# Kernel optimization log

Measured on AMD Instinct MI355X. Metric: run time of the kernel, lower is better.

The kernel has to match this reference:

```python
import jax, jax.numpy as jnp
import numpy as np

B, T, C, H = 2, 2048, 1024, 16
N = C // H
MISS_ROWS = 128


def _rwkv7_scan(q, w_log, k, v, a, b):
    # all [B,T,H,N] float32 (bf16-rounded). RWKV7 delta-rule recurrence:
    #   S_t = S_{t-1} * diag(exp(w_t)) + (S_{t-1} a_t) b_t^T + v_t k_t^T
    #   o_t = S_t q_t   (state S has shape [B,H,Nv,Nk]; decay along k-dim)
    Bq, Tq, Hq, Nq = q.shape

    def step(S, inp):
        q_t, w_t, k_t, v_t, a_t, b_t = inp
        ew = jnp.exp(w_t)  # decay in (0,1) since w_log = -exp(...) < 0
        sa = jnp.einsum('bhvi,bhi->bhv', S, a_t)
        S = S * ew[:, :, None, :] + sa[..., None] * b_t[:, :, None, :] + v_t[..., None] * k_t[:, :, None, :]
        o = jnp.einsum('bhvj,bhj->bhv', S, q_t)
        return S, o

    xs = tuple(jnp.moveaxis(u, 1, 0) for u in (q, w_log, k, v, a, b))
    S0 = jnp.zeros((Bq, Hq, Nq, Nq), jnp.float32)
    _, o = jax.lax.scan(step, S0, xs)
    return jnp.moveaxis(o, 0, 1)  # [B,T,H,N]


def setup_inputs() -> dict:
    key = jax.random.key(0)
    ks = jax.random.split(key, 16)
    f32 = jnp.float32
    return {
        'residual': jax.random.normal(ks[0], (B, T, C), f32),
        'x': jax.random.normal(ks[1], (B, T, C), f32),
        'x0': jax.random.normal(ks[2], (B, T, C), f32),
        'dx0': jax.random.normal(ks[3], (B, T, C), f32),
        'Wq': jax.random.normal(ks[4], (C, C), f32) * 0.02,
        'Wk': jax.random.normal(ks[5], (C, C), f32) * 0.02,
        'Wv': jax.random.normal(ks[6], (C, C), f32) * 0.02,
        'Wproj': jax.random.normal(ks[7], (C, C), f32) * 0.02,
        'x_q': jax.random.uniform(ks[8], (1, 1, C), f32),
        'x_k': jax.random.uniform(ks[9], (1, 1, C), f32),
        'x_v': jax.random.uniform(ks[10], (1, 1, C), f32),
        'v0': 0.7 + 0.1 * jax.random.normal(ks[11], (1, 1, C), f32),
        'w0': -3.0 + 0.5 * jax.random.normal(ks[12], (1, 1, C), f32),
        'a0': 0.1 * jax.random.normal(ks[13], (1, 1, C), f32),
        'miss': jax.random.normal(ks[14], (MISS_ROWS, 4 * C), f32) * 0.02,
        'r_k': 0.1 * jax.random.normal(ks[15], (H, N), f32),
    }


def reference(residual, x, x0, dx0, Wq, Wk, Wv, Wproj, x_q, x_k, x_v, v0, w0, a0, miss, r_k):
    Bx, Tx, Cx = x.shape
    Hh, Nn = r_k.shape
    # token shift: dx_prev = x_{t-1} - x_t (zero-padded at t=0)
    dx_prev = jnp.concatenate([jnp.zeros_like(x[:, :1]), x[:, :-1]], axis=1) - x
    q = (x + dx_prev * x_q) @ Wq.T
    k = (x + dx_prev * x_k) @ Wk.T
    v = (x + dx_prev * x_v) @ Wv.T
    deltas = x[:, :, :miss.shape[0]] @ miss  # [B,T,4C]
    w_delta, v_delta, a_delta, g = jnp.split(deltas, 4, axis=-1)
    log_neglog_w = -jax.nn.softplus(-(w0 + w_delta)) - 0.5
    log_w = -jnp.exp(log_neglog_w)  # log decay, always < 0
    v_first = (x0 + dx0 * x_v) @ Wv.T
    v = v + (v_first - v) * jax.nn.sigmoid(v0 + v_delta)
    g = 1.0 + g
    a = jax.nn.sigmoid(a0 + a_delta)
    kh = k.reshape(Bx, Tx, Hh, Nn)
    kk = kh / jnp.maximum(jnp.linalg.norm(kh, axis=-1, keepdims=True), 1e-12)
    kk = kk.reshape(Bx, Tx, Cx)
    k = k * a
    z = -kk
    b = kk * a
    bf = lambda u: u.astype(jnp.bfloat16).astype(jnp.float32).reshape(Bx, Tx, Hh, Nn)
    qh, wh, kh2, vh, zh, bh = (bf(u) for u in (q, log_w, k, v, z, b))
    y = _rwkv7_scan(qh, wh, kh2, vh, zh, bh) * (float(Nn) ** -0.5)  # [B,T,H,N]
    xnorm = jnp.linalg.norm(x.reshape(Bx, Tx, Hh, Nn), axis=-1, keepdims=True)
    vnorm = jnp.linalg.norm(vh, axis=-1, keepdims=True)
    u = (1.0 - xnorm / (vnorm + 1e-12)) * jax.nn.sigmoid(r_k)
    y = (y + vh * u).reshape(Bx, Tx, Cx)
    y = y * g
    return residual + y @ Wproj.T
```

## Files before the change

### kernel.cpp

```cpp
#include <hip/hip_runtime.h>
#include <stdint.h>
#include <stddef.h>

#define B_ 2
#define T_ 2048
#define C_ 1024
#define H_ 16
#define N_ 64
#define M_ (B_*T_)
#define L_ 128
#define NC_ (T_/L_)

typedef unsigned short ushort_t;
typedef __attribute__((ext_vector_type(8))) __bf16 bf16x8;
typedef __attribute__((ext_vector_type(4))) float  f32x4;

__device__ __forceinline__ ushort_t f2bf(float x){
  uint32_t u = __float_as_uint(x);
  u += 0x7fffu + ((u >> 16) & 1u);
  return (ushort_t)(u >> 16);
}
__device__ __forceinline__ float bf2f(uint32_t hu){
  return __uint_as_float(hu << 16);
}

__device__ __forceinline__ ushort4 mixq4(float4 a, float4 p, float4 c){
  ushort4 o;
  o.x = f2bf(fmaf(p.x - a.x, c.x, a.x));
  o.y = f2bf(fmaf(p.y - a.y, c.y, a.y));
  o.z = f2bf(fmaf(p.z - a.z, c.z, a.z));
  o.w = f2bf(fmaf(p.w - a.w, c.w, a.w));
  return o;
}
__global__ __launch_bounds__(256) void prep_act(
    const float* __restrict__ x, const float* __restrict__ x0,
    const float* __restrict__ dx0,
    const float* __restrict__ xq, const float* __restrict__ xk,
    const float* __restrict__ xv,
    ushort_t* __restrict__ Aq, ushort_t* __restrict__ Ak,
    ushort_t* __restrict__ Av, ushort_t* __restrict__ Axf,
    ushort_t* __restrict__ Xb)
{
  const int idx = blockIdx.x*256 + threadIdx.x;
  const int col4 = idx & 255;
  const int i = idx >> 8;
  const int t = i & (T_-1);
  float4 a = ((const float4*)x)[idx];
  float4 p = {0.f,0.f,0.f,0.f};
  if (t > 0) p = ((const float4*)x)[idx - 256];
  float4 cq = ((const float4*)xq)[col4];
  float4 ck = ((const float4*)xk)[col4];
  float4 cv = ((const float4*)xv)[col4];
  ((ushort4*)Aq)[idx] = mixq4(a, p, cq);
  ((ushort4*)Ak)[idx] = mixq4(a, p, ck);
  ((ushort4*)Av)[idx] = mixq4(a, p, cv);
  float4 z = ((const float4*)x0)[idx];
  float4 d = ((const float4*)dx0)[idx];
  ushort4 of;
  of.x = f2bf(fmaf(d.x, cv.x, z.x));
  of.y = f2bf(fmaf(d.y, cv.y, z.y));
  of.z = f2bf(fmaf(d.z, cv.z, z.z));
  of.w = f2bf(fmaf(d.w, cv.w, z.w));
  ((ushort4*)Axf)[idx] = of;
  ushort4 ob = {f2bf(a.x), f2bf(a.y), f2bf(a.z), f2bf(a.w)};
  ((ushort4*)Xb)[idx] = ob;
}

__global__ __launch_bounds__(256) void prep_w(
    const float* __restrict__ Wq, const float* __restrict__ Wk,
    const float* __restrict__ Wv, const float* __restrict__ Wp,
    ushort_t* __restrict__ Wb, ushort_t* __restrict__ Wpb)
{
  const int y = blockIdx.y;
  const float* src = (y==0)?Wq:(y==1)?Wk:(y<4)?Wv:Wp;
  ushort_t* dst = (y<4) ? Wb + (size_t)y*C_*C_ : Wpb;
  const int idx = blockIdx.x*256 + threadIdx.x;
  float4 v = ((const float4*)src)[idx];
  ushort4 o = {f2bf(v.x), f2bf(v.y), f2bf(v.z), f2bf(v.w)};
  ((ushort4*)dst)[idx] = o;
}

__global__ __launch_bounds__(256) void prep_missT(
    const float* __restrict__ miss, ushort_t* __restrict__ missT)
{
  __shared__ ushort_t tile[128][66];
  const int j0 = blockIdx.x*64;
  const int tid = threadIdx.x;
#pragma unroll
  for (int rep=0; rep<8; rep++){
    int k = rep*16 + (tid>>4);
    int jj = (tid&15)*4;
    float4 v = *(const float4*)&miss[(size_t)k*4096 + j0 + jj];
    tile[k][jj+0]=f2bf(v.x); tile[k][jj+1]=f2bf(v.y);
    tile[k][jj+2]=f2bf(v.z); tile[k][jj+3]=f2bf(v.w);
  }
  __syncthreads();
#pragma unroll
  for (int rep=0; rep<8; rep++){
    int j = tid>>2;
    int kk = (tid&3)*32 + rep*4;
    ushort4 o = {tile[kk+0][j], tile[kk+1][j], tile[kk+2][j], tile[kk+3][j]};
    *(ushort4*)&missT[(size_t)(j0+j)*128 + kk] = o;
  }
}

__global__ __launch_bounds__(256, 2) void mfma_gemm(
    const ushort_t* __restrict__ Ab, int lda, int64_t Asz,
    const ushort_t* __restrict__ Bbp, int ldb, int64_t Bsz,
    void* __restrict__ Cb, int ldc, int64_t Csz, int c_bf16,
    const float* __restrict__ resid, int K)
{
  const ushort_t* A  = Ab  + (size_t)blockIdx.z * Asz;
  const ushort_t* Bm = Bbp + (size_t)blockIdx.z * Bsz;
  const int i0 = blockIdx.y * 128;
  const int j0 = blockIdx.x * 128;
  const int tid = threadIdx.x;
  const int lane = tid & 63;
  const int w = tid >> 6;
  const int wm = w & 1, wn = w >> 1;

  __shared__ ushort_t As[128*32];
  __shared__ ushort_t Bs[128*32];

  f32x4 acc[4][4];
#pragma unroll
  for (int i=0;i<4;i++)
#pragma unroll
    for (int j=0;j<4;j++) acc[i][j] = (f32x4){0.f,0.f,0.f,0.f};

  const int lr = lane >> 2;
  const int ls = lane & 3;
  const ushort_t* ga = A  + (size_t)(i0 + w*32 + lr)*lda + ls*8;
  const ushort_t* gb = Bm + (size_t)(j0 + w*32 + lr)*ldb + ls*8;
  const int lm = lane & 15, lq = lane >> 4;

  for (int k0 = 0; k0 < K; k0 += 32){
    __syncthreads();
#pragma unroll
    for (int p=0;p<2;p++){
      __builtin_amdgcn_global_load_lds(
        (const __attribute__((address_space(1))) void*)(ga + (size_t)p*16*lda + k0),
        (__attribute__((address_space(3))) void*)&As[(w*32 + p*16)*32], 16, 0, 0);
      __builtin_amdgcn_global_load_lds(
        (const __attribute__((address_space(1))) void*)(gb + (size_t)p*16*ldb + k0),
        (__attribute__((address_space(3))) void*)&Bs[(w*32 + p*16)*32], 16, 0, 0);
    }
    __syncthreads();
    bf16x8 af[4], bfr[4];
#pragma unroll
    for (int i=0;i<4;i++)
      af[i] = *(const bf16x8*)&As[(wm*64 + i*16 + lm)*32 + lq*8];
#pragma unroll
    for (int j=0;j<4;j++)
      bfr[j] = *(const bf16x8*)&Bs[(wn*64 + j*16 + lm)*32 + lq*8];
#pragma unroll
    for (int i=0;i<4;i++)
#pragma unroll
      for (int j=0;j<4;j++)
        acc[i][j] = __builtin_amdgcn_mfma_f32_16x16x32_bf16(af[i], bfr[j], acc[i][j], 0, 0, 0);
  }

  if (!c_bf16){
    float* C = (float*)Cb + (size_t)blockIdx.z * Csz;
#pragma unroll
    for (int i=0;i<4;i++)
#pragma unroll
      for (int j=0;j<4;j++)
#pragma unroll
        for (int r=0;r<4;r++){
          const int row = i0 + wm*64 + i*16 + lq*4 + r;
          const int col = j0 + wn*64 + j*16 + lm;
          float v = acc[i][j][r];
          if (resid) v += resid[(size_t)row*ldc + col];
          C[(size_t)row*ldc + col] = v;
        }
  } else {
    ushort_t* C = (ushort_t*)Cb + (size_t)blockIdx.z * Csz;
#pragma unroll
    for (int i=0;i<4;i++)
#pragma unroll
      for (int j=0;j<4;j++)
#pragma unroll
        for (int r=0;r<4;r++){
          const int row = i0 + wm*64 + i*16 + lq*4 + r;
          const int col = j0 + wn*64 + j*16 + lm;
          C[(size_t)row*ldc + col] = f2bf(acc[i][j][r]);
        }
  }
}

__global__ __launch_bounds__(256) void fuse_kernel(
    const float* __restrict__ qm, const float* __restrict__ km,
    const float* __restrict__ vm, const float* __restrict__ vfm,
    const ushort_t* __restrict__ del, const float* __restrict__ x,
    const float* __restrict__ w0, const float* __restrict__ v0,
    const float* __restrict__ a0,
    uint32_t* __restrict__ packed, float* __restrict__ gout,
    float* __restrict__ ratio)
{
  const int lane = threadIdx.x & 63;
  const int ht = blockIdx.x*4 + (threadIdx.x >> 6);
  const int i = ht >> 4;
  const int h = ht & 15;
  const int c = h*64 + lane;
  const size_t ic = (size_t)i*C_ + c;
  float qv = qm[ic], kv = km[ic], vv = vm[ic], vfv = vfm[ic], xv = x[ic];
  const size_t d0 = (size_t)i*4*C_ + c;
  float wd = bf2f(del[d0]), vd = bf2f(del[d0+C_]);
  float ad = bf2f(del[d0+2*C_]), gd = bf2f(del[d0+3*C_]);

  float z1 = -(w0[c]+wd);
  float sp = fmaxf(z1, 0.f) + log1pf(expf(-fabsf(z1)));
  float logw = -expf(-sp - 0.5f);
  float sv = 1.f/(1.f+expf(-(v0[c]+vd)));
  vv = vv + (vfv - vv)*sv;
  float gv = 1.f + gd;
  float av = 1.f/(1.f+expf(-(a0[c]+ad)));

  ushort_t vr_u = f2bf(vv);
  float vrf = bf2f(vr_u);

  float ksq = kv*kv, xsq = xv*xv, vsq = vrf*vrf;
#pragma unroll
  for (int off=32; off>0; off>>=1){
    ksq += __shfl_xor(ksq, off, 64);
    xsq += __shfl_xor(xsq, off, 64);
    vsq += __shfl_xor(vsq, off, 64);
  }
  float kn = sqrtf(ksq);
  float kkn = kv / fmaxf(kn, 1e-12f);
  float k2 = kv*av;
  float zv = -kkn;
  float bv = kkn*av;

  uint32_t p0 = (uint32_t)f2bf(logw) | ((uint32_t)f2bf(zv) << 16);
  uint32_t p1 = (uint32_t)f2bf(bv)   | ((uint32_t)f2bf(k2) << 16);
  uint32_t p2 = (uint32_t)f2bf(qv)   | ((uint32_t)vr_u << 16);
  uint32_t* pb = packed + ((size_t)ht*64 + lane)*3;
  pb[0]=p0; pb[1]=p1; pb[2]=p2;
  gout[ic] = gv;
  if (lane == 0)
    ratio[ht] = 1.f - sqrtf(xsq)/(sqrtf(vsq)+1e-12f);
}


__global__ __launch_bounds__(256) void chunk_phi_kernel(
    const uint32_t* __restrict__ packed,
    float* __restrict__ phi, float* __restrict__ cc)
{
  const int blk = blockIdx.x;
  const int c  = blk & (NC_-1);
  const int bh = blk >> 4;
  const int b = bh >> 4, h = bh & 15;
  const int tid = threadIdx.x;
  const int rp = tid >> 2;
  const int qr = tid & 3;
  const int t0 = c * L_;

  __shared__ float ewS[4][N_], zS[4][N_], bS[4][N_], kS[4][N_], vS[4][N_];

  float X[16], Z[16];
#pragma unroll
  for (int i=0;i<16;i++){ X[i] = (qr*16+i == rp) ? 1.f : 0.f; Z[i] = 0.f; }

  const int s = tid >> 6, d = tid & 63;
  size_t ap = (((size_t)(b*T_+t0+s))*H_ + h)*64 + d;
  uint32_t pu0 = packed[ap*3], pu1 = packed[ap*3+1], pu2 = packed[ap*3+2];

  for (int tg = 0; tg < L_; tg += 4){
    __syncthreads();
    ewS[s][d] = __expf(bf2f(pu0 & 0xffffu));
    zS[s][d]  = bf2f(pu0 >> 16);
    bS[s][d]  = bf2f(pu1 & 0xffffu);
    kS[s][d]  = bf2f(pu1 >> 16);
    vS[s][d]  = bf2f(pu2 >> 16);
    if (tg + 4 < L_){
      size_t a2 = (((size_t)(b*T_+t0+tg+4+s))*H_ + h)*64 + d;
      pu0 = packed[a2*3]; pu1 = packed[a2*3+1]; pu2 = packed[a2*3+2];
    }
    __syncthreads();
#pragma unroll 1
    for (int ss=0; ss<4; ss++){
      float4 zv[4], ev[4], bv4[4], kv[4];
#pragma unroll
      for (int i4=0;i4<4;i4++){
        zv[i4]  = *(const float4*)&zS[ss][qr*16+i4*4];
        ev[i4]  = *(const float4*)&ewS[ss][qr*16+i4*4];
        bv4[i4] = *(const float4*)&bS[ss][qr*16+i4*4];
        kv[i4]  = *(const float4*)&kS[ss][qr*16+i4*4];
      }
      const float vr = vS[ss][rp];
      float a0=0.f,a1=0.f,a2=0.f,a3=0.f, c0=0.f,c1=0.f,c2=0.f,c3=0.f;
#pragma unroll
      for (int i4=0;i4<4;i4++){
        const float4 z4 = zv[i4];
        a0 = fmaf(X[i4*4+0], z4.x, a0); a1 = fmaf(X[i4*4+1], z4.y, a1);
        a2 = fmaf(X[i4*4+2], z4.z, a2); a3 = fmaf(X[i4*4+3], z4.w, a3);
        c0 = fmaf(Z[i4*4+0], z4.x, c0); c1 = fmaf(Z[i4*4+1], z4.y, c1);
        c2 = fmaf(Z[i4*4+2], z4.z, c2); c3 = fmaf(Z[i4*4+3], z4.w, c3);
      }
      float sx = (a0+a1)+(a2+a3);
      float sz = (c0+c1)+(c2+c3);
      sx += __shfl_xor(sx,1,64); sx += __shfl_xor(sx,2,64);
      sz += __shfl_xor(sz,1,64); sz += __shfl_xor(sz,2,64);
#pragma unroll
      for (int i4=0;i4<4;i4++){
        const float4 e4=ev[i4], b4=bv4[i4], k4=kv[i4];
        X[i4*4+0] = fmaf(X[i4*4+0], e4.x, sx*b4.x);
        X[i4*4+1] = fmaf(X[i4*4+1], e4.y, sx*b4.y);
        X[i4*4+2] = fmaf(X[i4*4+2], e4.z, sx*b4.z);
        X[i4*4+3] = fmaf(X[i4*4+3], e4.w, sx*b4.w);
        Z[i4*4+0] = fmaf(Z[i4*4+0], e4.x, fmaf(sz, b4.x, vr*k4.x));
        Z[i4*4+1] = fmaf(Z[i4*4+1], e4.y, fmaf(sz, b4.y, vr*k4.y));
        Z[i4*4+2] = fmaf(Z[i4*4+2], e4.z, fmaf(sz, b4.z, vr*k4.z));
        Z[i4*4+3] = fmaf(Z[i4*4+3], e4.w, fmaf(sz, b4.w, vr*k4.w));
      }
    }
  }
  const size_t base = (size_t)blk*4096 + (size_t)rp*64 + qr*16;
#pragma unroll
  for (int i4=0;i4<4;i4++){
    float4 xo = {X[i4*4+0],X[i4*4+1],X[i4*4+2],X[i4*4+3]};
    float4 zo = {Z[i4*4+0],Z[i4*4+1],Z[i4*4+2],Z[i4*4+3]};
    *(float4*)&phi[base + i4*4] = xo;
    *(float4*)&cc [base + i4*4] = zo;
  }
}

__global__ __launch_bounds__(256) void chunk_state_kernel(
    const float* __restrict__ phi, const float* __restrict__ cc,
    float* __restrict__ sstart)
{
  const int bh = blockIdx.x;
  const int tid = threadIdx.x;
  const int rb = tid >> 4;
  const int cq = tid & 15;
  __shared__ float Sld[64][65];
  __shared__ float Fld[64][68];
  float acc[4][4];
#pragma unroll
  for (int m=0;m<4;m++)
#pragma unroll
    for (int i=0;i<4;i++) acc[m][i] = 0.f;
#pragma unroll
  for (int m=0;m<4;m++){
    float4 z4 = {0.f,0.f,0.f,0.f};
    *(float4*)&Sld[rb+16*m][cq*4] = z4;
  }
  const float* pc = phi + (size_t)bh*NC_*4096;
  float4 pf[4];
#pragma unroll
  for (int p=0;p<4;p++) pf[p] = *(const float4*)&pc[(size_t)p*1024 + tid*4];

  for (int c=0;c<NC_;c++){
    __syncthreads();
#pragma unroll
    for (int p=0;p<4;p++){
      int f = p*1024 + tid*4;
      *(float4*)&Fld[f>>6][f&63] = pf[p];
    }
    if (c+1 < NC_){
#pragma unroll
      for (int p=0;p<4;p++) pf[p] = *(const float4*)&pc[(size_t)(c+1)*4096 + p*1024 + tid*4];
    }
    float na[4][4];
#pragma unroll
    for (int m=0;m<4;m++){
      float4 ci = *(const float4*)&cc[(size_t)(bh*NC_+c)*4096 + (size_t)(rb+16*m)*64 + cq*4];
      na[m][0]=ci.x; na[m][1]=ci.y; na[m][2]=ci.z; na[m][3]=ci.w;
    }
#pragma unroll
    for (int m=0;m<4;m++){
      float4 so = {acc[m][0],acc[m][1],acc[m][2],acc[m][3]};
      *(float4*)&sstart[(size_t)(bh*NC_+c)*4096 + (size_t)(rb+16*m)*64 + cq*4] = so;
    }
    __syncthreads();
#pragma unroll 1
    for (int k0=0;k0<64;k0+=4){
      float4 sr[4];
#pragma unroll
      for (int m=0;m<4;m++) sr[m] = *(const float4*)&Sld[rb+16*m][k0];
      const float4 f0 = *(const float4*)&Fld[k0+0][cq*4];
      const float4 f1 = *(const float4*)&Fld[k0+1][cq*4];
      const float4 f2 = *(const float4*)&Fld[k0+2][cq*4];
      const float4 f3 = *(const float4*)&Fld[k0+3][cq*4];
#pragma unroll
      for (int m=0;m<4;m++){
        na[m][0] = fmaf(sr[m].x, f0.x, na[m][0]); na[m][0] = fmaf(sr[m].y, f1.x, na[m][0]);
        na[m][0] = fmaf(sr[m].z, f2.x, na[m][0]); na[m][0] = fmaf(sr[m].w, f3.x, na[m][0]);
        na[m][1] = fmaf(sr[m].x, f0.y, na[m][1]); na[m][1] = fmaf(sr[m].y, f1.y, na[m][1]);
        na[m][1] = fmaf(sr[m].z, f2.y, na[m][1]); na[m][1] = fmaf(sr[m].w, f3.y, na[m][1]);
        na[m][2] = fmaf(sr[m].x, f0.z, na[m][2]); na[m][2] = fmaf(sr[m].y, f1.z, na[m][2]);
        na[m][2] = fmaf(sr[m].z, f2.z, na[m][2]); na[m][2] = fmaf(sr[m].w, f3.z, na[m][2]);
        na[m][3] = fmaf(sr[m].x, f0.w, na[m][3]); na[m][3] = fmaf(sr[m].y, f1.w, na[m][3]);
        na[m][3] = fmaf(sr[m].z, f2.w, na[m][3]); na[m][3] = fmaf(sr[m].w, f3.w, na[m][3]);
      }
    }
    __syncthreads();
#pragma unroll
    for (int m=0;m<4;m++){
      float4 so = {na[m][0],na[m][1],na[m][2],na[m][3]};
      *(float4*)&Sld[rb+16*m][cq*4] = so;
#pragma unroll
      for (int i=0;i<4;i++) acc[m][i] = na[m][i];
    }
  }
}

__global__ __launch_bounds__(256) void chunk_out_kernel(
    const uint32_t* __restrict__ packed, const float* __restrict__ ratio,
    const float* __restrict__ g, const float* __restrict__ rk,
    const float* __restrict__ sstart, ushort_t* __restrict__ y)
{
  const int blk = blockIdx.x;
  const int c  = blk & (NC_-1);
  const int bh = blk >> 4;
  const int b = bh >> 4, h = bh & 15;
  const int tid = threadIdx.x;
  const int r  = tid >> 2;
  const int qr = tid & 3;
  const int t0 = c * L_;

  __shared__ float ewS[4][N_], zS[4][N_], bS[4][N_], kS[4][N_], qS[4][N_], vS[4][N_], gS[4][N_];
  __shared__ float ratS[4];

  float S[16];
#pragma unroll
  for (int i4=0;i4<4;i4++){
    float4 s4 = *(const float4*)&sstart[(size_t)blk*4096 + (size_t)r*64 + qr*16 + i4*4];
    S[i4*4+0]=s4.x; S[i4*4+1]=s4.y; S[i4*4+2]=s4.z; S[i4*4+3]=s4.w;
  }
  const float sigrk = 1.f/(1.f+__expf(-rk[h*64+r]));

  const int s = tid >> 6, d = tid & 63;
  size_t ap = (((size_t)(b*T_+t0+s))*H_ + h)*64 + d;
  uint32_t pu0 = packed[ap*3], pu1 = packed[ap*3+1], pu2 = packed[ap*3+2];
  float pg = g[(size_t)(b*T_+t0+s)*C_ + h*64 + d];
  float prat = 0.f;
  if (d == 0) prat = ratio[(size_t)(b*T_+t0+s)*H_ + h];

  for (int tg = 0; tg < L_; tg += 4){
    __syncthreads();
    ewS[s][d] = __expf(bf2f(pu0 & 0xffffu));
    zS[s][d]  = bf2f(pu0 >> 16);
    bS[s][d]  = bf2f(pu1 & 0xffffu);
    kS[s][d]  = bf2f(pu1 >> 16);
    qS[s][d]  = bf2f(pu2 & 0xffffu);
    vS[s][d]  = bf2f(pu2 >> 16);
    gS[s][d]  = pg;
    if (d == 0) ratS[s] = prat;
    if (tg + 4 < L_){
      size_t a2 = (((size_t)(b*T_+t0+tg+4+s))*H_ + h)*64 + d;
      pu0 = packed[a2*3]; pu1 = packed[a2*3+1]; pu2 = packed[a2*3+2];
      pg = g[(size_t)(b*T_+t0+tg+4+s)*C_ + h*64 + d];
      if (d == 0) prat = ratio[(size_t)(b*T_+t0+tg+4+s)*H_ + h];
    }
    __syncthreads();
#pragma unroll 1
    for (int ss=0; ss<4; ss++){
      float4 zv[4], ev[4], bv4[4], kv[4], qv[4];
#pragma unroll
      for (int i4=0;i4<4;i4++){
        zv[i4]  = *(const float4*)&zS[ss][qr*16+i4*4];
        ev[i4]  = *(const float4*)&ewS[ss][qr*16+i4*4];
        bv4[i4] = *(const float4*)&bS[ss][qr*16+i4*4];
        kv[i4]  = *(const float4*)&kS[ss][qr*16+i4*4];
        qv[i4]  = *(const float4*)&qS[ss][qr*16+i4*4];
      }
      const float vr = vS[ss][r];
      const float gvr = gS[ss][r];
      const float uv = ratS[ss];
      float a0=0.f,a1=0.f,a2=0.f,a3=0.f;
#pragma unroll
      for (int i4=0;i4<4;i4++){
        const float4 z4 = zv[i4];
        a0 = fmaf(S[i4*4+0], z4.x, a0); a1 = fmaf(S[i4*4+1], z4.y, a1);
        a2 = fmaf(S[i4*4+2], z4.z, a2); a3 = fmaf(S[i4*4+3], z4.w, a3);
      }
      float sa = (a0+a1)+(a2+a3);
      sa += __shfl_xor(sa,1,64); sa += __shfl_xor(sa,2,64);
      float p0=0.f,p1=0.f,p2=0.f,p3=0.f;
#pragma unroll
      for (int i4=0;i4<4;i4++){
        const float4 e4=ev[i4], b4=bv4[i4], k4=kv[i4], q4=qv[i4];
        float t;
        t = fmaf(S[i4*4+0], e4.x, fmaf(sa, b4.x, vr*k4.x)); S[i4*4+0]=t; p0 = fmaf(t, q4.x, p0);
        t = fmaf(S[i4*4+1], e4.y, fmaf(sa, b4.y, vr*k4.y)); S[i4*4+1]=t; p1 = fmaf(t, q4.y, p1);
        t = fmaf(S[i4*4+2], e4.z, fmaf(sa, b4.z, vr*k4.z)); S[i4*4+2]=t; p2 = fmaf(t, q4.z, p2);
        t = fmaf(S[i4*4+3], e4.w, fmaf(sa, b4.w, vr*k4.w)); S[i4*4+3]=t; p3 = fmaf(t, q4.w, p3);
      }
      float o = (p0+p1)+(p2+p3);
      o += __shfl_xor(o,1,64); o += __shfl_xor(o,2,64);
      if (qr == 0){
        y[(size_t)(b*T_+t0+tg+ss)*C_ + h*64 + r] = f2bf((o*0.125f + vr*uv*sigrk)*gvr);
      }
    }
  }
}

extern "C" void kernel_launch(void* const* d_in, const int* in_sizes, int n_in,
                              void* d_out, int out_size, void* d_ws, size_t ws_size,
                              hipStream_t stream)
{
  const float* residual = (const float*)d_in[0];
  const float* x    = (const float*)d_in[1];
  const float* x0   = (const float*)d_in[2];
  const float* dx0  = (const float*)d_in[3];
  const float* Wq   = (const float*)d_in[4];
  const float* Wk   = (const float*)d_in[5];
  const float* Wv   = (const float*)d_in[6];
  const float* Wpr  = (const float*)d_in[7];
  const float* x_q  = (const float*)d_in[8];
  const float* x_k  = (const float*)d_in[9];
  const float* x_v  = (const float*)d_in[10];
  const float* v0   = (const float*)d_in[11];
  const float* w0   = (const float*)d_in[12];
  const float* a0   = (const float*)d_in[13];
  const float* miss = (const float*)d_in[14];
  const float* rk   = (const float*)d_in[15];
  float* out = (float*)d_out;

  char* ws = (char*)d_ws;
  const size_t MB = (size_t)1 << 20;
  float*    q_m    = (float*)(ws + 0*MB);
  float*    k_m    = (float*)(ws + 16*MB);
  float*    v_m    = (float*)(ws + 32*MB);
  float*    vf_m   = (float*)(ws + 48*MB);
  ushort_t* delb   = (ushort_t*)(ws + 64*MB);
  float*    phi    = (float*)(ws + 96*MB);
  float*    cc     = (float*)(ws + 104*MB);
  float*    sstart = (float*)(ws + 112*MB);
  ushort_t* Wpb    = (ushort_t*)(ws + 120*MB);
  ushort_t* missT  = (ushort_t*)(ws + 122*MB);
  ushort_t* Ab     = (ushort_t*)(ws + 124*MB);
  ushort_t* Xb     = (ushort_t*)(ws + 156*MB);
  ushort_t* Wb     = (ushort_t*)(ws + 164*MB);
  uint32_t* packed = (uint32_t*)(ws + 124*MB);
  float*    g_m    = (float*)(ws + 172*MB);
  float*    ratio  = (float*)(ws + 188*MB);
  ushort_t* yb     = (ushort_t*)(ws + 0*MB);

  ushort_t* Aq  = Ab + 0*(size_t)M_*C_;
  ushort_t* Ak  = Ab + 1*(size_t)M_*C_;
  ushort_t* Av  = Ab + 2*(size_t)M_*C_;
  ushort_t* Axf = Ab + 3*(size_t)M_*C_;

  dim3 blk(256);
  prep_act<<<M_*C_/4/256, blk, 0, stream>>>(x, x0, dx0, x_q, x_k, x_v, Aq, Ak, Av, Axf, Xb);
  prep_w<<<dim3(C_*C_/4/256, 5), blk, 0, stream>>>(Wq, Wk, Wv, Wpr, Wb, Wpb);
  prep_missT<<<4096/64, blk, 0, stream>>>(miss, missT);
  mfma_gemm<<<dim3(C_/128, M_/128, 4), blk, 0, stream>>>(
      Ab, C_, (int64_t)M_*C_, Wb, C_, (int64_t)C_*C_,
      q_m, C_, (int64_t)M_*C_, 0, nullptr, C_);
  mfma_gemm<<<dim3(4*C_/128, M_/128, 1), blk, 0, stream>>>(
      Xb, C_, 0, missT, 128, 0, delb, 4*C_, 0, 1, nullptr, 128);
  fuse_kernel<<<M_*H_/4, blk, 0, stream>>>(q_m, k_m, v_m, vf_m, delb, x, w0, v0, a0, packed, g_m, ratio);
  chunk_phi_kernel<<<B_*H_*NC_, blk, 0, stream>>>(packed, phi, cc);
  chunk_state_kernel<<<B_*H_, blk, 0, stream>>>(phi, cc, sstart);
  chunk_out_kernel<<<B_*H_*NC_, blk, 0, stream>>>(packed, ratio, g_m, rk, sstart, yb);
  mfma_gemm<<<dim3(C_/128, M_/128, 1), blk, 0, stream>>>(
      yb, C_, 0, Wpb, C_, 0, out, C_, 0, 0, residual, C_);
}
```

Baseline: 531.0 us.

## Precompute chunk-local output projections so emit pass is parallel dot products

The chunk pass now also records, per timestep, the projections of the affine state maps onto q (md buffer). The output stage becomes an embarrassingly parallel dot product of the chunk start state with these vectors, replacing the second sequential recurrence. The chunk length is halved to give more parallel blocks, and the three prep kernels are merged into one launch. The cost is extra global traffic for the md buffer and a longer sequential state-propagation chain across twice as many chunks.

```diff
diff --git a/kernel.cpp b/kernel.cpp
--- a/kernel.cpp
+++ b/kernel.cpp
@@ -8,7 +8,7 @@
 #define H_ 16
 #define N_ 64
 #define M_ (B_*T_)
-#define L_ 128
+#define L_ 64
 #define NC_ (T_/L_)
 
 typedef unsigned short ushort_t;
@@ -32,75 +32,73 @@
   o.w = f2bf(fmaf(p.w - a.w, c.w, a.w));
   return o;
 }
-__global__ __launch_bounds__(256) void prep_act(
+__global__ __launch_bounds__(256) void prep_all(
     const float* __restrict__ x, const float* __restrict__ x0,
     const float* __restrict__ dx0,
     const float* __restrict__ xq, const float* __restrict__ xk,
     const float* __restrict__ xv,
+    const float* __restrict__ Wq, const float* __restrict__ Wk,
+    const float* __restrict__ Wv, const float* __restrict__ Wp,
+    const float* __restrict__ miss,
     ushort_t* __restrict__ Aq, ushort_t* __restrict__ Ak,
     ushort_t* __restrict__ Av, ushort_t* __restrict__ Axf,
-    ushort_t* __restrict__ Xb)
-{
-  const int idx = blockIdx.x*256 + threadIdx.x;
-  const int col4 = idx & 255;
-  const int i = idx >> 8;
-  const int t = i & (T_-1);
-  float4 a = ((const float4*)x)[idx];
-  float4 p = {0.f,0.f,0.f,0.f};
-  if (t > 0) p = ((const float4*)x)[idx - 256];
-  float4 cq = ((const float4*)xq)[col4];
-  float4 ck = ((const float4*)xk)[col4];
-  float4 cv = ((const float4*)xv)[col4];
-  ((ushort4*)Aq)[idx] = mixq4(a, p, cq);
-  ((ushort4*)Ak)[idx] = mixq4(a, p, ck);
-  ((ushort4*)Av)[idx] = mixq4(a, p, cv);
-  float4 z = ((const float4*)x0)[idx];
-  float4 d = ((const float4*)dx0)[idx];
-  ushort4 of;
-  of.x = f2bf(fmaf(d.x, cv.x, z.x));
-  of.y = f2bf(fmaf(d.y, cv.y, z.y));
-  of.z = f2bf(fmaf(d.z, cv.z, z.z));
-  of.w = f2bf(fmaf(d.w, cv.w, z.w));
-  ((ushort4*)Axf)[idx] = of;
-  ushort4 ob = {f2bf(a.x), f2bf(a.y), f2bf(a.z), f2bf(a.w)};
-  ((ushort4*)Xb)[idx] = ob;
-}
-
-__global__ __launch_bounds__(256) void prep_w(
-    const float* __restrict__ Wq, const float* __restrict__ Wk,
-    const float* __restrict__ Wv, const float* __restrict__ Wp,
-    ushort_t* __restrict__ Wb, ushort_t* __restrict__ Wpb)
-{
-  const int y = blockIdx.y;
-  const float* src = (y==0)?Wq:(y==1)?Wk:(y<4)?Wv:Wp;
-  ushort_t* dst = (y<4) ? Wb + (size_t)y*C_*C_ : Wpb;
-  const int idx = blockIdx.x*256 + threadIdx.x;
-  float4 v = ((const float4*)src)[idx];
-  ushort4 o = {f2bf(v.x), f2bf(v.y), f2bf(v.z), f2bf(v.w)};
-  ((ushort4*)dst)[idx] = o;
-}
-
-__global__ __launch_bounds__(256) void prep_missT(
-    const float* __restrict__ miss, ushort_t* __restrict__ missT)
+    ushort_t* __restrict__ Xb,
+    ushort_t* __restrict__ Wb, ushort_t* __restrict__ Wpb,
+    ushort_t* __restrict__ missT)
 {
   __shared__ ushort_t tile[128][66];
-  const int j0 = blockIdx.x*64;
+  const int blk = blockIdx.x;
   const int tid = threadIdx.x;
-#pragma unroll
-  for (int rep=0; rep<8; rep++){
-    int k = rep*16 + (tid>>4);
-    int jj = (tid&15)*4;
-    float4 v = *(const float4*)&miss[(size_t)k*4096 + j0 + jj];
-    tile[k][jj+0]=f2bf(v.x); tile[k][jj+1]=f2bf(v.y);
-    tile[k][jj+2]=f2bf(v.z); tile[k][jj+3]=f2bf(v.w);
-  }
-  __syncthreads();
-#pragma unroll
-  for (int rep=0; rep<8; rep++){
-    int j = tid>>2;
-    int kk = (tid&3)*32 + rep*4;
-    ushort4 o = {tile[kk+0][j], tile[kk+1][j], tile[kk+2][j], tile[kk+3][j]};
-    *(ushort4*)&missT[(size_t)(j0+j)*128 + kk] = o;
+  if (blk < 4096){
+    const int idx = blk*256 + tid;
+    const int col4 = idx & 255;
+    const int i = idx >> 8;
+    const int t = i & (T_-1);
+    float4 a = ((const float4*)x)[idx];
+    float4 p = {0.f,0.f,0.f,0.f};
+    if (t > 0) p = ((const float4*)x)[idx - 256];
+    float4 cq = ((const float4*)xq)[col4];
+    float4 ck = ((const float4*)xk)[col4];
+    float4 cv = ((const float4*)xv)[col4];
+    ((ushort4*)Aq)[idx] = mixq4(a, p, cq);
+    ((ushort4*)Ak)[idx] = mixq4(a, p, ck);
+    ((ushort4*)Av)[idx] = mixq4(a, p, cv);
+    float4 z = ((const float4*)x0)[idx];
+    float4 d = ((const float4*)dx0)[idx];
+    ushort4 of;
+    of.x = f2bf(fmaf(d.x, cv.x, z.x));
+    of.y = f2bf(fmaf(d.y, cv.y, z.y));
+    of.z = f2bf(fmaf(d.z, cv.z, z.z));
+    of.w = f2bf(fmaf(d.w, cv.w, z.w));
+    ((ushort4*)Axf)[idx] = of;
+    ushort4 ob = {f2bf(a.x), f2bf(a.y), f2bf(a.z), f2bf(a.w)};
+    ((ushort4*)Xb)[idx] = ob;
+  } else if (blk < 4096 + 5*1024){
+    const int y = (blk - 4096) >> 10;
+    const float* src = (y==0)?Wq:(y==1)?Wk:(y<4)?Wv:Wp;
+    ushort_t* dst = (y<4) ? Wb + (size_t)y*C_*C_ : Wpb;
+    const int idx = ((blk - 4096) & 1023)*256 + tid;
+    float4 v = ((const float4*)src)[idx];
+    ushort4 o = {f2bf(v.x), f2bf(v.y), f2bf(v.z), f2bf(v.w)};
+    ((ushort4*)dst)[idx] = o;
+  } else {
+    const int j0 = (blk - 4096 - 5*1024)*64;
+#pragma unroll
+    for (int rep=0; rep<8; rep++){
+      int k = rep*16 + (tid>>4);
+      int jj = (tid&15)*4;
+      float4 v = *(const float4*)&miss[(size_t)k*4096 + j0 + jj];
+      tile[k][jj+0]=f2bf(v.x); tile[k][jj+1]=f2bf(v.y);
+      tile[k][jj+2]=f2bf(v.z); tile[k][jj+3]=f2bf(v.w);
+    }
+    __syncthreads();
+#pragma unroll
+    for (int rep=0; rep<8; rep++){
+      int j = tid>>2;
+      int kk = (tid&3)*32 + rep*4;
+      ushort4 o = {tile[kk+0][j], tile[kk+1][j], tile[kk+2][j], tile[kk+3][j]};
+      *(ushort4*)&missT[(size_t)(j0+j)*128 + kk] = o;
+    }
   }
 }
 
@@ -244,20 +242,20 @@
 }
 
 
-__global__ __launch_bounds__(256) void chunk_phi_kernel(
+__global__ __launch_bounds__(256) void chunk_mdp_kernel(
     const uint32_t* __restrict__ packed,
-    float* __restrict__ phi, float* __restrict__ cc)
+    float* __restrict__ phi, float* __restrict__ cc, float* __restrict__ md)
 {
   const int blk = blockIdx.x;
   const int c  = blk & (NC_-1);
-  const int bh = blk >> 4;
+  const int bh = blk >> 5;
   const int b = bh >> 4, h = bh & 15;
   const int tid = threadIdx.x;
   const int rp = tid >> 2;
   const int qr = tid & 3;
   const int t0 = c * L_;
 
-  __shared__ float ewS[4][N_], zS[4][N_], bS[4][N_], kS[4][N_], vS[4][N_];
+  __shared__ float ewS[4][N_], zS[4][N_], bS[4][N_], kS[4][N_], qS[4][N_], vS[4][N_];
 
   float X[16], Z[16];
 #pragma unroll
@@ -273,6 +271,7 @@
     zS[s][d]  = bf2f(pu0 >> 16);
     bS[s][d]  = bf2f(pu1 & 0xffffu);
     kS[s][d]  = bf2f(pu1 >> 16);
+    qS[s][d]  = bf2f(pu2 & 0xffffu);
     vS[s][d]  = bf2f(pu2 >> 16);
     if (tg + 4 < L_){
       size_t a2 = (((size_t)(b*T_+t0+tg+4+s))*H_ + h)*64 + d;
@@ -281,13 +280,14 @@
     __syncthreads();
 #pragma unroll 1
     for (int ss=0; ss<4; ss++){
-      float4 zv[4], ev[4], bv4[4], kv[4];
+      float4 zv[4], ev[4], bv4[4], kv[4], qv[4];
 #pragma unroll
       for (int i4=0;i4<4;i4++){
         zv[i4]  = *(const float4*)&zS[ss][qr*16+i4*4];
         ev[i4]  = *(const float4*)&ewS[ss][qr*16+i4*4];
         bv4[i4] = *(const float4*)&bS[ss][qr*16+i4*4];
         kv[i4]  = *(const float4*)&kS[ss][qr*16+i4*4];
+        qv[i4]  = *(const float4*)&qS[ss][qr*16+i4*4];
       }
       const float vr = vS[ss][rp];
       float a0=0.f,a1=0.f,a2=0.f,a3=0.f, c0=0.f,c1=0.f,c2=0.f,c3=0.f;
@@ -303,18 +303,26 @@
       float sz = (c0+c1)+(c2+c3);
       sx += __shfl_xor(sx,1,64); sx += __shfl_xor(sx,2,64);
       sz += __shfl_xor(sz,1,64); sz += __shfl_xor(sz,2,64);
+      float m0=0.f,m1=0.f,m2=0.f,m3=0.f, d0=0.f,d1=0.f,d2=0.f,d3=0.f;
 #pragma unroll
       for (int i4=0;i4<4;i4++){
-        const float4 e4=ev[i4], b4=bv4[i4], k4=kv[i4];
-        X[i4*4+0] = fmaf(X[i4*4+0], e4.x, sx*b4.x);
-        X[i4*4+1] = fmaf(X[i4*4+1], e4.y, sx*b4.y);
-        X[i4*4+2] = fmaf(X[i4*4+2], e4.z, sx*b4.z);
-        X[i4*4+3] = fmaf(X[i4*4+3], e4.w, sx*b4.w);
-        Z[i4*4+0] = fmaf(Z[i4*4+0], e4.x, fmaf(sz, b4.x, vr*k4.x));
-        Z[i4*4+1] = fmaf(Z[i4*4+1], e4.y, fmaf(sz, b4.y, vr*k4.y));
-        Z[i4*4+2] = fmaf(Z[i4*4+2], e4.z, fmaf(sz, b4.z, vr*k4.z));
-        Z[i4*4+3] = fmaf(Z[i4*4+3], e4.w, fmaf(sz, b4.w, vr*k4.w));
+        const float4 e4=ev[i4], b4=bv4[i4], k4=kv[i4], q4=qv[i4];
+        float t;
+        t = fmaf(X[i4*4+0], e4.x, sx*b4.x); X[i4*4+0]=t; m0 = fmaf(t, q4.x, m0);
+        t = fmaf(X[i4*4+1], e4.y, sx*b4.y); X[i4*4+1]=t; m1 = fmaf(t, q4.y, m1);
+        t = fmaf(X[i4*4+2], e4.z, sx*b4.z); X[i4*4+2]=t; m2 = fmaf(t, q4.z, m2);
+        t = fmaf(X[i4*4+3], e4.w, sx*b4.w); X[i4*4+3]=t; m3 = fmaf(t, q4.w, m3);
+        t = fmaf(Z[i4*4+0], e4.x, fmaf(sz, b4.x, vr*k4.x)); Z[i4*4+0]=t; d0 = fmaf(t, q4.x, d0);
+        t = fmaf(Z[i4*4+1], e4.y, fmaf(sz, b4.y, vr*k4.y)); Z[i4*4+1]=t; d1 = fmaf(t, q4.y, d1);
+        t = fmaf(Z[i4*4+2], e4.z, fmaf(sz, b4.z, vr*k4.z)); Z[i4*4+2]=t; d2 = fmaf(t, q4.z, d2);
+        t = fmaf(Z[i4*4+3], e4.w, fmaf(sz, b4.w, vr*k4.w)); Z[i4*4+3]=t; d3 = fmaf(t, q4.w, d3);
       }
+      float mv = (m0+m1)+(m2+m3);
+      float dv = (d0+d1)+(d2+d3);
+      mv += __shfl_xor(mv,1,64); mv += __shfl_xor(mv,2,64);
+      dv += __shfl_xor(dv,1,64); dv += __shfl_xor(dv,2,64);
+      if (qr == 0)      md[((size_t)blk*L_ + tg+ss)*128 + rp]      = mv;
+      else if (qr == 1) md[((size_t)blk*L_ + tg+ss)*128 + 64 + rp] = dv;
     }
   }
   const size_t base = (size_t)blk*4096 + (size_t)rp*64 + qr*16;
@@ -407,94 +415,48 @@
   }
 }
 
-__global__ __launch_bounds__(256) void chunk_out_kernel(
+__global__ __launch_bounds__(256) void chunk_emit_kernel(
     const uint32_t* __restrict__ packed, const float* __restrict__ ratio,
     const float* __restrict__ g, const float* __restrict__ rk,
-    const float* __restrict__ sstart, ushort_t* __restrict__ y)
+    const float* __restrict__ sstart, const float* __restrict__ md,
+    ushort_t* __restrict__ y)
 {
   const int blk = blockIdx.x;
   const int c  = blk & (NC_-1);
-  const int bh = blk >> 4;
+  const int bh = blk >> 5;
   const int b = bh >> 4, h = bh & 15;
   const int tid = threadIdx.x;
-  const int r  = tid >> 2;
-  const int qr = tid & 3;
-  const int t0 = c * L_;
-
-  __shared__ float ewS[4][N_], zS[4][N_], bS[4][N_], kS[4][N_], qS[4][N_], vS[4][N_], gS[4][N_];
-  __shared__ float ratS[4];
-
-  float S[16];
-#pragma unroll
-  for (int i4=0;i4<4;i4++){
-    float4 s4 = *(const float4*)&sstart[(size_t)blk*4096 + (size_t)r*64 + qr*16 + i4*4];
-    S[i4*4+0]=s4.x; S[i4*4+1]=s4.y; S[i4*4+2]=s4.z; S[i4*4+3]=s4.w;
-  }
-  const float sigrk = 1.f/(1.f+__expf(-rk[h*64+r]));
-
-  const int s = tid >> 6, d = tid & 63;
-  size_t ap = (((size_t)(b*T_+t0+s))*H_ + h)*64 + d;
-  uint32_t pu0 = packed[ap*3], pu1 = packed[ap*3+1], pu2 = packed[ap*3+2];
-  float pg = g[(size_t)(b*T_+t0+s)*C_ + h*64 + d];
-  float prat = 0.f;
-  if (d == 0) prat = ratio[(size_t)(b*T_+t0+s)*H_ + h];
-
-  for (int tg = 0; tg < L_; tg += 4){
-    __syncthreads();
-    ewS[s][d] = __expf(bf2f(pu0 & 0xffffu));
-    zS[s][d]  = bf2f(pu0 >> 16);
-    bS[s][d]  = bf2f(pu1 & 0xffffu);
-    kS[s][d]  = bf2f(pu1 >> 16);
-    qS[s][d]  = bf2f(pu2 & 0xffffu);
-    vS[s][d]  = bf2f(pu2 >> 16);
-    gS[s][d]  = pg;
-    if (d == 0) ratS[s] = prat;
-    if (tg + 4 < L_){
-      size_t a2 = (((size_t)(b*T_+t0+tg+4+s))*H_ + h)*64 + d;
-      pu0 = packed[a2*3]; pu1 = packed[a2*3+1]; pu2 = packed[a2*3+2];
-      pg = g[(size_t)(b*T_+t0+tg+4+s)*C_ + h*64 + d];
-      if (d == 0) prat = ratio[(size_t)(b*T_+t0+tg+4+s)*H_ + h];
-    }
-    __syncthreads();
+  const int v = tid & 63;
+  const int tg = tid >> 6;
+
+  float4 sr[16];
+  const float4* sp = (const float4*)(sstart + (size_t)blk*4096 + (size_t)v*64);
+#pragma unroll
+  for (int f=0;f<16;f++) sr[f] = sp[f];
+  const float sigrk = 1.f/(1.f+__expf(-rk[h*64+v]));
+
 #pragma unroll 1
-    for (int ss=0; ss<4; ss++){
-      float4 zv[4], ev[4], bv4[4], kv[4], qv[4];
-#pragma unroll
-      for (int i4=0;i4<4;i4++){
-        zv[i4]  = *(const float4*)&zS[ss][qr*16+i4*4];
-        ev[i4]  = *(const float4*)&ewS[ss][qr*16+i4*4];
-        bv4[i4] = *(const float4*)&bS[ss][qr*16+i4*4];
-        kv[i4]  = *(const float4*)&kS[ss][qr*16+i4*4];
-        qv[i4]  = *(const float4*)&qS[ss][qr*16+i4*4];
-      }
-      const float vr = vS[ss][r];
-      const float gvr = gS[ss][r];
-      const float uv = ratS[ss];
-      float a0=0.f,a1=0.f,a2=0.f,a3=0.f;
-#pragma unroll
-      for (int i4=0;i4<4;i4++){
-        const float4 z4 = zv[i4];
-        a0 = fmaf(S[i4*4+0], z4.x, a0); a1 = fmaf(S[i4*4+1], z4.y, a1);
-        a2 = fmaf(S[i4*4+2], z4.z, a2); a3 = fmaf(S[i4*4+3], z4.w, a3);
-      }
-      float sa = (a0+a1)+(a2+a3);
-      sa += __shfl_xor(sa,1,64); sa += __shfl_xor(sa,2,64);
-      float p0=0.f,p1=0.f,p2=0.f,p3=0.f;
-#pragma unroll
-      for (int i4=0;i4<4;i4++){
-        const float4 e4=ev[i4], b4=bv4[i4], k4=kv[i4], q4=qv[i4];
-        float t;
-        t = fmaf(S[i4*4+0], e4.x, fmaf(sa, b4.x, vr*k4.x)); S[i4*4+0]=t; p0 = fmaf(t, q4.x, p0);
-        t = fmaf(S[i4*4+1], e4.y, fmaf(sa, b4.y, vr*k4.y)); S[i4*4+1]=t; p1 = fmaf(t, q4.y, p1);
-        t = fmaf(S[i4*4+2], e4.z, fmaf(sa, b4.z, vr*k4.z)); S[i4*4+2]=t; p2 = fmaf(t, q4.z, p2);
-        t = fmaf(S[i4*4+3], e4.w, fmaf(sa, b4.w, vr*k4.w)); S[i4*4+3]=t; p3 = fmaf(t, q4.w, p3);
-      }
-      float o = (p0+p1)+(p2+p3);
-      o += __shfl_xor(o,1,64); o += __shfl_xor(o,2,64);
-      if (qr == 0){
-        y[(size_t)(b*T_+t0+tg+ss)*C_ + h*64 + r] = f2bf((o*0.125f + vr*uv*sigrk)*gvr);
-      }
-    }
+  for (int ss=0; ss<16; ss++){
+    const int t = tg*16 + ss;
+    const int token = b*T_ + c*L_ + t;
+    const float* mrow = md + ((size_t)blk*L_ + t)*128;
+    float o0=0.f,o1=0.f,o2=0.f,o3=0.f;
+#pragma unroll
+    for (int f=0;f<16;f+=4){
+      float4 m0 = ((const float4*)mrow)[f+0];
+      float4 m1 = ((const float4*)mrow)[f+1];
+      float4 m2 = ((const float4*)mrow)[f+2];
+      float4 m3 = ((const float4*)mrow)[f+3];
+      o0 = fmaf(sr[f+0].x,m0.x, fmaf(sr[f+0].y,m0.y, fmaf(sr[f+0].z,m0.z, fmaf(sr[f+0].w,m0.w, o0))));
+      o1 = fmaf(sr[f+1].x,m1.x, fmaf(sr[f+1].y,m1.y, fmaf(sr[f+1].z,m1.z, fmaf(sr[f+1].w,m1.w, o1))));
+      o2 = fmaf(sr[f+2].x,m2.x, fmaf(sr[f+2].y,m2.y, fmaf(sr[f+2].z,m2.z, fmaf(sr[f+2].w,m2.w, o2))));
+      o3 = fmaf(sr[f+3].x,m3.x, fmaf(sr[f+3].y,m3.y, fmaf(sr[f+3].z,m3.z, fmaf(sr[f+3].w,m3.w, o3))));
+    }
+    float o = ((o0+o1)+(o2+o3)) + mrow[64 + v];
+    const float vt = bf2f(packed[(((size_t)token*H_ + h)*64 + v)*3 + 2] >> 16);
+    const float uv = ratio[(size_t)token*H_ + h];
+    const float gv = g[(size_t)token*C_ + h*64 + v];
+    y[(size_t)token*C_ + h*64 + v] = f2bf((o*0.125f + vt*uv*sigrk)*gv);
   }
 }
 
@@ -527,18 +489,19 @@
   float*    v_m    = (float*)(ws + 32*MB);
   float*    vf_m   = (float*)(ws + 48*MB);
   ushort_t* delb   = (ushort_t*)(ws + 64*MB);
-  float*    phi    = (float*)(ws + 96*MB);
-  float*    cc     = (float*)(ws + 104*MB);
-  float*    sstart = (float*)(ws + 112*MB);
-  ushort_t* Wpb    = (ushort_t*)(ws + 120*MB);
-  ushort_t* missT  = (ushort_t*)(ws + 122*MB);
-  ushort_t* Ab     = (ushort_t*)(ws + 124*MB);
-  ushort_t* Xb     = (ushort_t*)(ws + 156*MB);
-  ushort_t* Wb     = (ushort_t*)(ws + 164*MB);
-  uint32_t* packed = (uint32_t*)(ws + 124*MB);
-  float*    g_m    = (float*)(ws + 172*MB);
-  float*    ratio  = (float*)(ws + 188*MB);
-  ushort_t* yb     = (ushort_t*)(ws + 0*MB);
+  ushort_t* Ab     = (ushort_t*)(ws + 96*MB);
+  ushort_t* Xb     = (ushort_t*)(ws + 128*MB);
+  ushort_t* Wb     = (ushort_t*)(ws + 136*MB);
+  uint32_t* packed = (uint32_t*)(ws + 96*MB);
+  float*    g_m    = (float*)(ws + 144*MB);
+  ushort_t* Wpb    = (ushort_t*)(ws + 160*MB);
+  ushort_t* missT  = (ushort_t*)(ws + 162*MB);
+  float*    ratio  = (float*)(ws + 163*MB);
+  float*    phi    = (float*)(ws + 0*MB);
+  float*    cc     = (float*)(ws + 16*MB);
+  float*    sstart = (float*)(ws + 32*MB);
+  ushort_t* yb     = (ushort_t*)(ws + 48*MB);
+  float*    mdbuf  = (float*)(ws + 64*MB);
 
   ushort_t* Aq  = Ab + 0*(size_t)M_*C_;
   ushort_t* Ak  = Ab + 1*(size_t)M_*C_;
@@ -546,18 +509,18 @@
   ushort_t* Axf = Ab + 3*(size_t)M_*C_;
 
   dim3 blk(256);
-  prep_act<<<M_*C_/4/256, blk, 0, stream>>>(x, x0, dx0, x_q, x_k, x_v, Aq, Ak, Av, Axf, Xb);
-  prep_w<<<dim3(C_*C_/4/256, 5), blk, 0, stream>>>(Wq, Wk, Wv, Wpr, Wb, Wpb);
-  prep_missT<<<4096/64, blk, 0, stream>>>(miss, missT);
+  prep_all<<<4096 + 5*1024 + 64, blk, 0, stream>>>(
+      x, x0, dx0, x_q, x_k, x_v, Wq, Wk, Wv, Wpr, miss,
+      Aq, Ak, Av, Axf, Xb, Wb, Wpb, missT);
   mfma_gemm<<<dim3(C_/128, M_/128, 4), blk, 0, stream>>>(
       Ab, C_, (int64_t)M_*C_, Wb, C_, (int64_t)C_*C_,
       q_m, C_, (int64_t)M_*C_, 0, nullptr, C_);
   mfma_gemm<<<dim3(4*C_/128, M_/128, 1), blk, 0, stream>>>(
       Xb, C_, 0, missT, 128, 0, delb, 4*C_, 0, 1, nullptr, 128);
   fuse_kernel<<<M_*H_/4, blk, 0, stream>>>(q_m, k_m, v_m, vf_m, delb, x, w0, v0, a0, packed, g_m, ratio);
-  chunk_phi_kernel<<<B_*H_*NC_, blk, 0, stream>>>(packed, phi, cc);
+  chunk_mdp_kernel<<<B_*H_*NC_, blk, 0, stream>>>(packed, phi, cc, mdbuf);
   chunk_state_kernel<<<B_*H_, blk, 0, stream>>>(phi, cc, sstart);
-  chunk_out_kernel<<<B_*H_*NC_, blk, 0, stream>>>(packed, ratio, g_m, rk, sstart, yb);
+  chunk_emit_kernel<<<B_*H_*NC_, blk, 0, stream>>>(packed, ratio, g_m, rk, sstart, mdbuf, yb);
   mfma_gemm<<<dim3(C_/128, M_/128, 1), blk, 0, stream>>>(
       yb, C_, 0, Wpb, C_, 0, out, C_, 0, 0, residual, C_);
 }
```

Result: slower. 587.6 us (+10.7%).
